# Optimization experiments

Hardware: AMD Instinct MI355X
Metric: run time of the kernel (lower is better)

Reference implementation:

```python
import jax, jax.numpy as jnp
import numpy as np

IN, OUT, RANK, ALPHA, NSUB = 4096, 4096, 16, 32, 4
SCALING = ALPHA / RANK


def setup_inputs() -> dict:
    key = jax.random.key(0)
    ks = jax.random.split(key, 8)
    B, S = 4, 2048
    return {
        "x": jax.random.normal(ks[0], (B, S, IN), dtype=jnp.float32),
        "base_W": jax.random.normal(ks[1], (OUT, IN), dtype=jnp.float32) * 0.02,
        "base_b": jax.random.normal(ks[2], (OUT,), dtype=jnp.float32) * 0.02,
        "base_A": jax.random.normal(ks[3], (RANK, IN), dtype=jnp.float32) * 0.02,
        "base_B": jax.random.normal(ks[4], (OUT, RANK), dtype=jnp.float32) * 0.02,
        "sub_wgate": jax.random.normal(ks[5], (NSUB, IN), dtype=jnp.float32) * 0.02,
        "sub_A": jax.random.normal(ks[6], (NSUB, RANK, IN), dtype=jnp.float32) * 0.02,
        "sub_B": jax.random.normal(ks[7], (NSUB, OUT, RANK), dtype=jnp.float32) * 0.02,
    }


def reference(x, base_W, base_b, base_A, base_B, sub_wgate, sub_A, sub_B):
    # base linear: [B,S,IN] @ [IN,OUT] + bias
    out = jnp.einsum("bsd,od->bso", x, base_W) + base_b
    # base LoRA: x @ A^T @ B^T
    out = out + SCALING * jnp.einsum("bsr,or->bso", jnp.einsum("bsd,rd->bsr", x, base_A), base_B)
    # stacked ReLU-gated sub-adapters, batched over adapter dim j
    gates = jax.nn.relu(jnp.einsum("bsd,jd->bsj", x, sub_wgate))        # [B,S,J]
    mid = jnp.einsum("bsd,jrd->bsjr", x, sub_A)                           # [B,S,J,R] (small)
    # gate * (mid @ B^T) == (gate*mid) @ B^T since gate is per-token scalar
    gated_mid = mid * gates[..., None]
    out = out + SCALING * jnp.einsum("bsjr,jor->bso", gated_mid, sub_B)
    return out
```

## Files before the change

### kernel.cpp

```cpp
#include <hip/hip_runtime.h>
#include <hip/hip_bf16.h>
#include <stdint.h>

#define DIN   4096
#define DOUT  4096
#define RANK  16
#define NSUB  4
#define MTOT  8192
#define LDK   4160
#define KTAIL 64
#define NV    80
#define KTILES 65

typedef __attribute__((ext_vector_type(8)))  short    short8;
typedef __attribute__((ext_vector_type(4)))  float    floatx4;
typedef __attribute__((ext_vector_type(8)))  unsigned short ushort8;
typedef __attribute__((ext_vector_type(4)))  unsigned short ushort4v;

static __device__ __forceinline__ unsigned short f2bf(float f) {
    unsigned int u = __float_as_uint(f);
    unsigned int r = (u + 0x7FFFu + ((u >> 16) & 1u)) >> 16;
    return (unsigned short)r;
}

static __device__ __forceinline__ void async_copy16(const unsigned short* g, unsigned short* l) {
    __builtin_amdgcn_global_load_lds(
        (const __attribute__((address_space(1))) unsigned int*)g,
        (__attribute__((address_space(3))) unsigned int*)l,
        16, 0, 0);
}

__global__ __launch_bounds__(256) void build_v_kernel(
    const float* __restrict__ sub_wgate,
    const float* __restrict__ sub_A,
    unsigned short* __restrict__ Vc)
{
    const int t = threadIdx.x;
    const int row = blockIdx.x;
    const float* src = (row < 64) ? (sub_A + (size_t)row * DIN)
                     : (row < 68) ? (sub_wgate + (size_t)(row - 64) * DIN)
                     : nullptr;
#pragma unroll
    for (int i = 0; i < 4; ++i) {
        int c4 = t + 256 * i;
        ushort4v v;
        if (src) {
            float4 a = ((const float4*)src)[c4];
            v[0] = f2bf(a.x); v[1] = f2bf(a.y); v[2] = f2bf(a.z); v[3] = f2bf(a.w);
        } else {
            v[0] = v[1] = v[2] = v[3] = 0;
        }
        *(ushort4v*)(Vc + (size_t)row * DIN + c4 * 4) = v;
    }
}

#define BXK 256
#define LDA 264
__global__ __launch_bounds__(256) void build_x_kernel(
    const float* __restrict__ x,
    const unsigned short* __restrict__ Vc,
    unsigned short* __restrict__ Xc)
{
    __shared__ char smem[(16 + NV) * LDA * 2];
    unsigned short* As = (unsigned short*)smem;
    unsigned short* Bs = As + 16 * LDA;
    float* Pp = (float*)smem;

    const int t  = threadIdx.x;
    const int l  = t & 63;
    const int w  = t >> 6;
    const int m0 = blockIdx.x * 16;
    const int lane16 = l & 15;
    const int kq     = (l >> 4) * 8;

    floatx4 acc[5] = {};

    for (int cc = 0; cc < DIN; cc += BXK) {
#pragma unroll
        for (int i = 0; i < 2; ++i) {
            int u8 = t + 256 * i;
            int tr = u8 >> 5;
            int c8 = u8 & 31;
            const float4* src = (const float4*)(x + (size_t)(m0 + tr) * DIN + cc + c8 * 8);
            float4 a = src[0], b = src[1];
            ushort8 v;
            v[0] = f2bf(a.x); v[1] = f2bf(a.y); v[2] = f2bf(a.z); v[3] = f2bf(a.w);
            v[4] = f2bf(b.x); v[5] = f2bf(b.y); v[6] = f2bf(b.z); v[7] = f2bf(b.w);
            *(ushort8*)&As[tr * LDA + c8 * 8] = v;
            *(ushort8*)(Xc + (size_t)(m0 + tr) * LDK + cc + c8 * 8) = v;
        }
#pragma unroll
        for (int i = 0; i < 10; ++i) {
            int idx = t + 256 * i;
            int vr  = idx >> 5;
            int c8  = idx & 31;
            ushort8 v = *(const ushort8*)(Vc + (size_t)vr * DIN + cc + c8 * 8);
            *(ushort8*)&Bs[vr * LDA + c8 * 8] = v;
        }
        __syncthreads();

#pragma unroll
        for (int s = 0; s < 2; ++s) {
            int ks = w * 2 + s;
            short8 af = *(const short8*)&As[lane16 * LDA + ks * 32 + kq];
#pragma unroll
            for (int n = 0; n < 5; ++n) {
                short8 bf = *(const short8*)&Bs[(n * 16 + lane16) * LDA + ks * 32 + kq];
                acc[n] = __builtin_amdgcn_mfma_f32_16x16x32_bf16(af, bf, acc[n], 0, 0, 0);
            }
        }
        __syncthreads();
    }

#pragma unroll
    for (int n = 0; n < 5; ++n)
#pragma unroll
        for (int r = 0; r < 4; ++r)
            Pp[(w * 16 + (l >> 4) * 4 + r) * NV + n * 16 + lane16] = acc[n][r];
    __syncthreads();

#pragma unroll
    for (int i = 0; i < 4; ++i) {
        int v  = t + 256 * i;
        int tr = v >> 6;
        int c  = v & 63;
        int j  = c >> 4;
        float ps = 0.f, gs = 0.f;
#pragma unroll
        for (int q = 0; q < 4; ++q) {
            ps += Pp[(q * 16 + tr) * NV + c];
            gs += Pp[(q * 16 + tr) * NV + 64 + j];
        }
        Xc[(size_t)(m0 + tr) * LDK + DIN + c] = f2bf(2.0f * fmaxf(gs, 0.f) * ps);
    }
}

__global__ __launch_bounds__(256) void build_w_kernel(
    const float* __restrict__ W,
    const float* __restrict__ base_A,
    const float* __restrict__ base_B,
    const float* __restrict__ sub_B,
    unsigned short* __restrict__ Wc)
{
    __shared__ float bBs[8 * RANK];

    const int t  = threadIdx.x;
    const int o0 = (blockIdx.x >> 2) * 8;
    const int cc = (blockIdx.x & 3) * 1024;
    const int q  = (cc >> 2) + t;

    if (t < 128) bBs[t] = 2.0f * base_B[(size_t)o0 * RANK + t];
    __syncthreads();

    float4 acc[8];
#pragma unroll
    for (int o = 0; o < 8; ++o)
        acc[o] = ((const float4*)(W + (size_t)(o0 + o) * DIN))[q];

#pragma unroll
    for (int r = 0; r < RANK; ++r) {
        float4 a = ((const float4*)(base_A + (size_t)r * DIN))[q];
#pragma unroll
        for (int o = 0; o < 8; ++o) {
            float s = bBs[o * RANK + r];
            acc[o].x += s * a.x; acc[o].y += s * a.y;
            acc[o].z += s * a.z; acc[o].w += s * a.w;
        }
    }

#pragma unroll
    for (int o = 0; o < 8; ++o) {
        ushort4v v;
        v[0] = f2bf(acc[o].x); v[1] = f2bf(acc[o].y);
        v[2] = f2bf(acc[o].z); v[3] = f2bf(acc[o].w);
        *(ushort4v*)(Wc + (size_t)(o0 + o) * LDK + q * 4) = v;
    }

    if ((blockIdx.x & 3) == 0) {
#pragma unroll
        for (int i = 0; i < 2; ++i) {
            int v = t + 256 * i;
            int o = v >> 6;
            int c = v & 63;
            int j = c >> 4;
            int r = c & 15;
            float s = sub_B[((size_t)j * DOUT + (o0 + o)) * RANK + r];
            Wc[(size_t)(o0 + o) * LDK + DIN + c] = f2bf(s);
        }
    }
}

#define BARM() asm volatile("s_barrier" ::: "memory")

#define LDA_(B,MH,I,S) (*(const short8*)((const char*)lds + (B)*32768 + (MH)*8192 + (I)*2048 + (aBy ^ ((S)*64))))
#define LDB_(B,J,S)    (*(const short8*)((const char*)lds + 65536 + (B)*32768 + (J)*2048 + (bBy ^ ((S)*64))))

#define STG(P, DST) do { async_copy16((P), (DST)); \
                         async_copy16((P) + (size_t)64 * LDK, (DST) + 4096); } while (0)
#define STAGE_A0(P,B) STG((P), &lds[(B)*16384 + tid*8])
#define STAGE_A1(P,B) STG((P), &lds[(B)*16384 + 8192 + tid*8])
#define STAGE_B0(P,B) STG((P), &lds[32768 + (B)*16384 + tid*8])
#define STAGE_B1(P,B) STG((P), &lds[32768 + (B)*16384 + 8192 + tid*8])

#define MFMA_HALF(MH, JLO) do { \
    _Pragma("unroll") for (int s_ = 0; s_ < 2; ++s_) \
    _Pragma("unroll") for (int i_ = 0; i_ < 4; ++i_) \
    _Pragma("unroll") for (int jj_ = 0; jj_ < 2; ++jj_) \
        acc[(MH)*4+i_][(JLO)+jj_] = __builtin_amdgcn_mfma_f32_16x16x32_bf16( \
            af[i_][s_], bb[(JLO)+jj_][s_], acc[(MH)*4+i_][(JLO)+jj_], 0, 0, 0); \
} while (0)

#define TILE_BODY(T, CUR) do { \
     \
    _Pragma("unroll") for (int i_ = 0; i_ < 4; ++i_) { \
        af[i_][0] = LDA_(CUR, 0, i_, 0); af[i_][1] = LDA_(CUR, 0, i_, 1); } \
    _Pragma("unroll") for (int j_ = 0; j_ < 2; ++j_) { \
        bb[j_][0] = LDB_(CUR, j_, 0); bb[j_][1] = LDB_(CUR, j_, 1); } \
    if ((T) + 1 < KTILES) { STAGE_A1(pA1, (CUR) ^ 1); } \
    pA1 += 64; \
    __builtin_amdgcn_s_setprio(1); MFMA_HALF(0, 0); __builtin_amdgcn_s_setprio(0); \
    BARM(); \
     \
    _Pragma("unroll") for (int j_ = 2; j_ < 4; ++j_) { \
        bb[j_][0] = LDB_(CUR, j_, 0); bb[j_][1] = LDB_(CUR, j_, 1); } \
    __builtin_amdgcn_s_setprio(1); MFMA_HALF(0, 2); __builtin_amdgcn_s_setprio(0); \
    BARM(); \
     \
    _Pragma("unroll") for (int i_ = 0; i_ < 4; ++i_) { \
        af[i_][0] = LDA_(CUR, 1, i_, 0); af[i_][1] = LDA_(CUR, 1, i_, 1); } \
    if ((T) + 2 < KTILES) { STAGE_B0(pB0, CUR); STAGE_B1(pB1, CUR); } \
    pB0 += 64; pB1 += 64; \
    BARM(); \
    if ((T) + 2 < KTILES) { STAGE_A0(pA0, CUR); } \
    pA0 += 64; \
    __builtin_amdgcn_s_setprio(1); MFMA_HALF(1, 0); MFMA_HALF(1, 2); __builtin_amdgcn_s_setprio(0); \
    if ((T) + 2 < KTILES)      { asm volatile("s_waitcnt vmcnt(6)" ::: "memory"); } \
    else if ((T) + 1 < KTILES) { asm volatile("s_waitcnt vmcnt(0)" ::: "memory"); } \
    BARM(); \
} while (0)

__global__ __launch_bounds__(512, 2) void gemm_kernel(
    const unsigned short* __restrict__ Xc,
    const unsigned short* __restrict__ Wc,
    const float* __restrict__ bias,
    float* __restrict__ out)
{
    __shared__ unsigned short lds[65536];

    const int tid = threadIdx.x;
    const int l   = tid & 63;
    const int wv  = tid >> 6;
    const int wm  = wv >> 2;
    const int wn  = wv & 3;
    const int lane16 = l & 15;
    const int g   = l >> 4;
    const int lx  = lane16 & 7;

    const int bid = blockIdx.x;
    const int wg  = (bid & 7) * 64 + (bid >> 3);
    const int m0  = (wg >> 4) * 256;
    const int n0  = (wg & 15) * 256;

    const int aBy = wm * 16384 + lane16 * 128 + ((g ^ lx) << 4);
    const int bBy = wn * 8192  + lane16 * 128 + ((g ^ lx) << 4);

    const int r0 = tid >> 3;
    const int c0 = (tid & 7) ^ (r0 & 7);
    const unsigned short* pA0 = Xc + (size_t)(m0 + r0) * LDK + c0 * 8;
    const unsigned short* pA1 = pA0 + (size_t)128 * LDK;
    const unsigned short* pB0 = Wc + (size_t)(n0 + r0) * LDK + c0 * 8;
    const unsigned short* pB1 = pB0 + (size_t)128 * LDK;

    floatx4 acc[8][4] = {};
    short8 af[4][2], bb[4][2];

    STAGE_B0(pB0, 0); STAGE_B1(pB1, 0); STAGE_A0(pA0, 0); STAGE_A1(pA1, 0);
    STAGE_B0(pB0 + 64, 1); STAGE_B1(pB1 + 64, 1); STAGE_A0(pA0 + 64, 1);
    pA1 += 64; pB0 += 128; pB1 += 128; pA0 += 128;
    asm volatile("s_waitcnt vmcnt(6)" ::: "memory");
    BARM();

    for (int t = 0; t < KTILES - 1; t += 2) {
        TILE_BODY(t, 0);
        TILE_BODY(t + 1, 1);
    }
    TILE_BODY(KTILES - 1, 0);

    const int row_l = g * 4;
#pragma unroll
    for (int j = 0; j < 4; ++j) {
        const int gcol = n0 + wn * 64 + j * 16 + lane16;
        const float bv = bias[gcol];
#pragma unroll
        for (int i = 0; i < 8; ++i) {
            const int grow = m0 + wm * 128 + i * 16 + row_l;
            size_t base = (size_t)grow * DOUT + gcol;
            out[base]            = acc[i][j][0] + bv;
            out[base + DOUT]     = acc[i][j][1] + bv;
            out[base + 2 * DOUT] = acc[i][j][2] + bv;
            out[base + 3 * DOUT] = acc[i][j][3] + bv;
        }
    }
}

extern "C" void kernel_launch(void* const* d_in, const int* in_sizes, int n_in,
                              void* d_out, int out_size, void* d_ws, size_t ws_size,
                              hipStream_t stream) {
    const float* x         = (const float*)d_in[0];
    const float* base_W    = (const float*)d_in[1];
    const float* base_b    = (const float*)d_in[2];
    const float* base_A    = (const float*)d_in[3];
    const float* base_B    = (const float*)d_in[4];
    const float* sub_wgate = (const float*)d_in[5];
    const float* sub_A     = (const float*)d_in[6];
    const float* sub_B     = (const float*)d_in[7];
    float* out = (float*)d_out;

    unsigned short* Xc = (unsigned short*)d_ws;
    unsigned short* Wc = Xc + (size_t)MTOT * LDK;
    unsigned short* Vc = Wc + (size_t)DOUT * LDK;

    build_v_kernel<<<NV, 256, 0, stream>>>(sub_wgate, sub_A, Vc);
    build_x_kernel<<<MTOT / 16, 256, 0, stream>>>(x, Vc, Xc);
    build_w_kernel<<<(DOUT / 8) * 4, 256, 0, stream>>>(base_W, base_A, base_B, sub_B, Wc);
    gemm_kernel<<<dim3(DOUT / 256 * (MTOT / 256)), 512, 0, stream>>>(Xc, Wc, base_b, out);
}
```

Before: 524.4 us.

## Split x build into a conversion pass and a pipelined async-copy tail kernel

The fused build_x kernel is replaced by two kernels. The first is a plain fp32-to-bf16 conversion of x. The second computes the gated sub-adapter tail columns from the converted bf16 Xc, using 32-row blocks, double-buffered async global-to-LDS copies, XOR-swizzled LDS layout and manual waitcnt/barrier scheduling. The goal is to hide memory latency in the tail projection and halve how often the V matrix is re-read. The cost is an extra pass that reads back the bf16 Xc and one more kernel launch.

```diff
diff --git a/kernel.cpp b/kernel.cpp
--- a/kernel.cpp
+++ b/kernel.cpp
@@ -54,73 +54,104 @@
     }
 }
 
-#define BXK 256
-#define LDA 264
-__global__ __launch_bounds__(256) void build_x_kernel(
+__global__ __launch_bounds__(256) void convert_x_kernel(
     const float* __restrict__ x,
+    unsigned short* __restrict__ Xc)
+{
+    const int t = threadIdx.x;
+    const int b = blockIdx.x;
+#pragma unroll
+    for (int i = 0; i < 4; ++i) {
+        const int row = b * 4 + i;
+        const float4* s = (const float4*)(x + (size_t)row * DIN + t * 16);
+        float4 a = s[0], b4 = s[1], c = s[2], d = s[3];
+        ushort8 v0, v1;
+        v0[0] = f2bf(a.x);  v0[1] = f2bf(a.y);  v0[2] = f2bf(a.z);  v0[3] = f2bf(a.w);
+        v0[4] = f2bf(b4.x); v0[5] = f2bf(b4.y); v0[6] = f2bf(b4.z); v0[7] = f2bf(b4.w);
+        v1[0] = f2bf(c.x);  v1[1] = f2bf(c.y);  v1[2] = f2bf(c.z);  v1[3] = f2bf(c.w);
+        v1[4] = f2bf(d.x);  v1[5] = f2bf(d.y);  v1[6] = f2bf(d.z);  v1[7] = f2bf(d.w);
+        unsigned short* o = Xc + (size_t)row * LDK + t * 16;
+        *(ushort8*)o       = v0;
+        *(ushort8*)(o + 8) = v1;
+    }
+}
+
+#define XS_STG(P) do { unsigned short* d_ = &lds[(P)*8192 + t*8]; \
+    _Pragma("unroll") for (int i_ = 0; i_ < 4; ++i_) \
+        async_copy16(pXs + (size_t)(8*i_) * LDK, d_ + i_*2048); } while (0)
+#define VS_STG(P) do { unsigned short* d_ = &lds[16384 + (P)*20480 + t*8]; \
+    _Pragma("unroll") for (int i_ = 0; i_ < 10; ++i_) \
+        async_copy16(pVs + (size_t)(8*i_) * DIN, d_ + i_*2048); } while (0)
+
+#define XT_MM(P, KB) do { \
+    short8 a0_ = *(const short8*)((const char*)lds + (P)*16384 + aB + (KB)); \
+    short8 a1_ = *(const short8*)((const char*)lds + (P)*16384 + 8192 + aB + (KB)); \
+    _Pragma("unroll") for (int n_ = 0; n_ < 5; ++n_) { \
+        short8 b_ = *(const short8*)((const char*)lds + 32768 + (P)*40960 + n_*8192 + aB + (KB)); \
+        acc[0][n_] = __builtin_amdgcn_mfma_f32_16x16x32_bf16(a0_, b_, acc[0][n_], 0, 0, 0); \
+        acc[1][n_] = __builtin_amdgcn_mfma_f32_16x16x32_bf16(a1_, b_, acc[1][n_], 0, 0, 0); } \
+} while (0)
+
+#define XT_ITER(P, WN, DOSTG) do { \
+    asm volatile("s_waitcnt vmcnt(" #WN ")" ::: "memory"); \
+    asm volatile("s_barrier" ::: "memory"); \
+    XT_MM(P, kb0); \
+    XT_MM(P, kb1); \
+    asm volatile("s_barrier" ::: "memory"); \
+    if (DOSTG) { XS_STG(P); VS_STG(P); } \
+    pXs += 256; pVs += 256; \
+} while (0)
+
+__global__ __launch_bounds__(256) void xtail_kernel(
     const unsigned short* __restrict__ Vc,
     unsigned short* __restrict__ Xc)
 {
-    __shared__ char smem[(16 + NV) * LDA * 2];
-    unsigned short* As = (unsigned short*)smem;
-    unsigned short* Bs = As + 16 * LDA;
-    float* Pp = (float*)smem;
-
-    const int t  = threadIdx.x;
-    const int l  = t & 63;
-    const int w  = t >> 6;
-    const int m0 = blockIdx.x * 16;
+    __shared__ __align__(16) unsigned short lds[57344];
+
+    const int t = threadIdx.x;
+    const int l = t & 63;
+    const int w = t >> 6;
     const int lane16 = l & 15;
-    const int kq     = (l >> 4) * 8;
-
-    floatx4 acc[5] = {};
-
-    for (int cc = 0; cc < DIN; cc += BXK) {
-#pragma unroll
-        for (int i = 0; i < 2; ++i) {
-            int u8 = t + 256 * i;
-            int tr = u8 >> 5;
-            int c8 = u8 & 31;
-            const float4* src = (const float4*)(x + (size_t)(m0 + tr) * DIN + cc + c8 * 8);
-            float4 a = src[0], b = src[1];
-            ushort8 v;
-            v[0] = f2bf(a.x); v[1] = f2bf(a.y); v[2] = f2bf(a.z); v[3] = f2bf(a.w);
-            v[4] = f2bf(b.x); v[5] = f2bf(b.y); v[6] = f2bf(b.z); v[7] = f2bf(b.w);
-            *(ushort8*)&As[tr * LDA + c8 * 8] = v;
-            *(ushort8*)(Xc + (size_t)(m0 + tr) * LDK + cc + c8 * 8) = v;
-        }
-#pragma unroll
-        for (int i = 0; i < 10; ++i) {
-            int idx = t + 256 * i;
-            int vr  = idx >> 5;
-            int c8  = idx & 31;
-            ushort8 v = *(const ushort8*)(Vc + (size_t)vr * DIN + cc + c8 * 8);
-            *(ushort8*)&Bs[vr * LDA + c8 * 8] = v;
-        }
-        __syncthreads();
-
-#pragma unroll
-        for (int s = 0; s < 2; ++s) {
-            int ks = w * 2 + s;
-            short8 af = *(const short8*)&As[lane16 * LDA + ks * 32 + kq];
-#pragma unroll
-            for (int n = 0; n < 5; ++n) {
-                short8 bf = *(const short8*)&Bs[(n * 16 + lane16) * LDA + ks * 32 + kq];
-                acc[n] = __builtin_amdgcn_mfma_f32_16x16x32_bf16(af, bf, acc[n], 0, 0, 0);
-            }
-        }
-        __syncthreads();
-    }
-
-#pragma unroll
-    for (int n = 0; n < 5; ++n)
-#pragma unroll
-        for (int r = 0; r < 4; ++r)
-            Pp[(w * 16 + (l >> 4) * 4 + r) * NV + n * 16 + lane16] = acc[n][r];
+    const int g = l >> 4;
+    const int lx2 = lane16 & 7;
+    const int m0 = blockIdx.x * 32;
+
+    const int srow = t >> 5;
+    const int scl  = (t & 31) ^ (srow & 7);
+    const unsigned short* pXs = Xc + (size_t)(m0 + srow) * LDK + scl * 8;
+    const unsigned short* pVs = Vc + (size_t)srow * DIN + scl * 8;
+
+    const int hk  = lx2 >> 2;
+    const int gx  = g ^ (lx2 & 3);
+    const int kb0 = (((2*w + 0) ^ hk) * 4 + gx) * 16;
+    const int kb1 = (((2*w + 1) ^ hk) * 4 + gx) * 16;
+    const int aB  = lane16 * 512;
+
+    floatx4 acc[2][5] = {};
+
+    XS_STG(0); VS_STG(0); pXs += 256; pVs += 256;
+    XS_STG(1); VS_STG(1); pXs += 256; pVs += 256;
+
+#pragma unroll 1
+    for (int c = 0; c < 14; c += 2) {
+        XT_ITER(0, 14, 1);
+        XT_ITER(1, 14, 1);
+    }
+    XT_ITER(0, 14, 0);
+    XT_ITER(1, 0, 0);
+
+    float* Pp = (float*)lds;
+#pragma unroll
+    for (int tm = 0; tm < 2; ++tm)
+#pragma unroll
+        for (int n = 0; n < 5; ++n)
+#pragma unroll
+            for (int r = 0; r < 4; ++r)
+                Pp[((w * 32) + tm * 16 + (l >> 4) * 4 + r) * 80 + n * 16 + lane16] = acc[tm][n][r];
     __syncthreads();
 
 #pragma unroll
-    for (int i = 0; i < 4; ++i) {
+    for (int i = 0; i < 8; ++i) {
         int v  = t + 256 * i;
         int tr = v >> 6;
         int c  = v & 63;
@@ -128,8 +159,8 @@
         float ps = 0.f, gs = 0.f;
 #pragma unroll
         for (int q = 0; q < 4; ++q) {
-            ps += Pp[(q * 16 + tr) * NV + c];
-            gs += Pp[(q * 16 + tr) * NV + 64 + j];
+            ps += Pp[(q * 32 + tr) * 80 + c];
+            gs += Pp[(q * 32 + tr) * 80 + 64 + j];
         }
         Xc[(size_t)(m0 + tr) * LDK + DIN + c] = f2bf(2.0f * fmaxf(gs, 0.f) * ps);
     }
@@ -321,7 +352,8 @@
     unsigned short* Vc = Wc + (size_t)DOUT * LDK;
 
     build_v_kernel<<<NV, 256, 0, stream>>>(sub_wgate, sub_A, Vc);
-    build_x_kernel<<<MTOT / 16, 256, 0, stream>>>(x, Vc, Xc);
+    convert_x_kernel<<<MTOT / 4, 256, 0, stream>>>(x, Xc);
+    xtail_kernel<<<MTOT / 32, 256, 0, stream>>>(Vc, Xc);
     build_w_kernel<<<(DOUT / 8) * 4, 256, 0, stream>>>(base_W, base_A, base_B, sub_B, Wc);
     gemm_kernel<<<dim3(DOUT / 256 * (MTOT / 256)), 512, 0, stream>>>(Xc, Wc, base_b, out);
 }
```

After: 530.3 us. About the same (+1.1%).
